# Performance work log

Hardware: AMD Instinct MI355X
Metric: run time of the kernel (lower is better)

The kernel has to match this reference:

```python
import jax, jax.numpy as jnp
import numpy as np

N = 100000   # nodes
E = 1600000  # edges (edge_index1)
F_IN = 53    # num_features_xd
D1 = 128     # output_dim1
D2 = 64      # output_dim2
G = 512      # graphs in batch


def setup_inputs() -> dict:
    key = jax.random.key(0)
    ks = jax.random.split(key, 16)
    kaiming = lambda k, fi, fo: jax.random.normal(k, (fi, fo), jnp.float32) * np.float32(np.sqrt(2.0 / fi))
    glorot = lambda k, fi, fo: jax.random.normal(k, (fi, fo), jnp.float32) * np.float32(np.sqrt(1.0 / fi))
    return {
        "x": jax.random.normal(ks[0], (N, F_IN), jnp.float32),
        "edge_inter": jax.random.randint(ks[1], (2, E), 0, N),
        "edge_intra": jax.random.randint(ks[2], (2, E), 0, N),
        "batch": jnp.sort(jax.random.randint(ks[3], (N,), 0, G)),
        "num_graphs": G,
        "w1": kaiming(ks[4], F_IN, D1), "b1": jnp.zeros((D1,), jnp.float32),
        "w2": kaiming(ks[5], D1, D2), "b2": jnp.zeros((D2,), jnp.float32),
        "gat_w": glorot(ks[6], D2, D2),
        "att_src": jax.random.normal(ks[7], (D2,), jnp.float32) * 0.1,
        "att_dst": jax.random.normal(ks[8], (D2,), jnp.float32) * 0.1,
        "gat_b": jnp.zeros((D2,), jnp.float32),
        "gcn_w": glorot(ks[9], D2, 2 * D2), "gcn_b": jnp.zeros((2 * D2,), jnp.float32),
        "fc1_w": glorot(ks[10], 2 * D2, 512), "fc1_b": jnp.zeros((512,), jnp.float32),
        "fc2_w": glorot(ks[11], 512, 256), "fc2_b": jnp.zeros((256,), jnp.float32),
        "out_w": glorot(ks[12], 256, 1), "out_b": jnp.zeros((1,), jnp.float32),
    }


def reference(x, edge_inter, edge_intra, batch, num_graphs,
              w1, b1, w2, b2, gat_w, att_src, att_dst, gat_b,
              gcn_w, gcn_b, fc1_w, fc1_b, fc2_w, fc2_b, out_w, out_b):
    n = x.shape[0]
    # node_embed: two dense layers + relu
    h = jax.nn.relu(x @ w1 + b1)
    h = jax.nn.relu(h @ w2 + b2)

    # add self-loops (PyG default for GATConv and GCNConv)
    loops = jnp.arange(n)
    src = jnp.concatenate([edge_inter[0], loops])  # message source j
    dst = jnp.concatenate([edge_inter[1], loops])  # message target i

    # ---- GATConv (heads=1): gather -> score -> edge softmax -> scatter ----
    hp = h @ gat_w                           # [N, D2]
    a_s = hp @ att_src                       # [N]
    a_d = hp @ att_dst                       # [N]
    e = jax.nn.leaky_relu(a_s[src] + a_d[dst], negative_slope=0.2)  # [E+N]
    emax = jax.ops.segment_max(e, dst, num_segments=n)
    ee = jnp.exp(e - emax[dst])
    denom = jax.ops.segment_sum(ee, dst, num_segments=n)
    alpha = ee / denom[dst]                  # edge softmax per target node
    h = jax.ops.segment_sum(alpha[:, None] * hp[src], dst, num_segments=n) + gat_b
    h = jax.nn.relu(h)

    # ---- GCNConv: symmetric-normalized sparse aggregation ----
    hw = h @ gcn_w                           # [N, 2*D2]
    deg = jax.ops.segment_sum(jnp.ones_like(e), dst, num_segments=n)
    d_inv = jnp.where(deg > 0, deg ** -0.5, 0.0)
    norm = d_inv[src] * d_inv[dst]           # [E+N]
    h = jax.ops.segment_sum(norm[:, None] * hw[src], dst, num_segments=n) + gcn_b
    h = jax.nn.relu(h)

    # ---- global max pool over graphs ----
    g = jax.ops.segment_max(h, batch, num_segments=num_graphs)
    g = jnp.maximum(g, 0.0)  # guard empty segments (-inf); h >= 0 after relu

    # ---- MLP head (dropout is identity in eval mode) ----
    z = jax.nn.relu(g @ fc1_w + fc1_b)
    z = jax.nn.relu(z @ fc2_w + fc2_b)
    return z @ out_w + out_b
```

## Files before the change

### kernel.cpp

```cpp
#include <hip/hip_runtime.h>
#include <hip/hip_bf16.h>

#define F_IN 53
#define D1   128
#define D2   64
#define D3   128
#define H1SZ 512
#define H2SZ 256

#define BUKSZ   256
#define BUKMAX  512
#define CAP     5120
#define PART_CH 4096

__global__ void k_vecproj(const float* __restrict__ gat_w,
                          const float* __restrict__ att_src,
                          const float* __restrict__ att_dst,
                          float* __restrict__ v_src, float* __restrict__ v_dst) {
    int k = threadIdx.x;
    float as = 0.f, ad = 0.f;
    #pragma unroll
    for (int c = 0; c < D2; ++c) {
        float w = gat_w[k * D2 + c];
        as = fmaf(w, att_src[c], as);
        ad = fmaf(w, att_dst[c], ad);
    }
    v_src[k] = as;
    v_dst[k] = ad;
}

__global__ __launch_bounds__(256) void k_embed(const float* __restrict__ x,
                                               const float* __restrict__ w1,
                                               const float* __restrict__ b1,
                                               const float* __restrict__ w2,
                                               const float* __restrict__ b2,
                                               const float* __restrict__ gat_w,
                                               const float* __restrict__ v_src,
                                               const float* __restrict__ v_dst,
                                               float* __restrict__ hp,
                                               float* __restrict__ a_s,
                                               float* __restrict__ a_d, int N) {
    __shared__ __align__(16) float xs[32][56];
    __shared__ __align__(16) float h1s[32][D1];
    __shared__ __align__(16) float h2s[32][D2];
    int tid = threadIdx.x;
    int n0 = blockIdx.x * 32;
    for (int i = tid; i < 32 * F_IN; i += 256) {
        int node = i / F_IN, kk = i - node * F_IN;
        xs[node][kk] = x[(size_t)n0 * F_IN + i];
    }
    __syncthreads();
    int c = tid & 63, grp = tid >> 6;
    int nb = grp * 8;
    {
        float acc0[8], acc1[8];
        float bb0 = b1[c], bb1 = b1[c + 64];
        #pragma unroll
        for (int j = 0; j < 8; ++j) { acc0[j] = bb0; acc1[j] = bb1; }
        #pragma unroll 1
        for (int kc = 0; kc < 13; ++kc) {
            int k4 = kc * 4;
            float wa0 = w1[(k4 + 0) * D1 + c];
            float wa1 = w1[(k4 + 1) * D1 + c];
            float wa2 = w1[(k4 + 2) * D1 + c];
            float wa3 = w1[(k4 + 3) * D1 + c];
            float wb0 = w1[(k4 + 0) * D1 + c + 64];
            float wb1 = w1[(k4 + 1) * D1 + c + 64];
            float wb2 = w1[(k4 + 2) * D1 + c + 64];
            float wb3 = w1[(k4 + 3) * D1 + c + 64];
            #pragma unroll
            for (int j = 0; j < 8; ++j) {
                float4 xv = *reinterpret_cast<const float4*>(&xs[nb + j][k4]);
                acc0[j] = fmaf(xv.x, wa0, acc0[j]);
                acc0[j] = fmaf(xv.y, wa1, acc0[j]);
                acc0[j] = fmaf(xv.z, wa2, acc0[j]);
                acc0[j] = fmaf(xv.w, wa3, acc0[j]);
                acc1[j] = fmaf(xv.x, wb0, acc1[j]);
                acc1[j] = fmaf(xv.y, wb1, acc1[j]);
                acc1[j] = fmaf(xv.z, wb2, acc1[j]);
                acc1[j] = fmaf(xv.w, wb3, acc1[j]);
            }
        }
        {
            float wa = w1[52 * D1 + c], wb = w1[52 * D1 + c + 64];
            #pragma unroll
            for (int j = 0; j < 8; ++j) {
                float xv = xs[nb + j][52];
                acc0[j] = fmaf(xv, wa, acc0[j]);
                acc1[j] = fmaf(xv, wb, acc1[j]);
            }
        }
        #pragma unroll
        for (int j = 0; j < 8; ++j) {
            h1s[nb + j][c]      = fmaxf(acc0[j], 0.f);
            h1s[nb + j][c + 64] = fmaxf(acc1[j], 0.f);
        }
    }
    float h2v[8];
    {
        float bb = b2[c];
        #pragma unroll
        for (int j = 0; j < 8; ++j) h2v[j] = bb;
        #pragma unroll 1
        for (int kc = 0; kc < 32; ++kc) {
            int k4 = kc * 4;
            float w0 = w2[(k4 + 0) * D2 + c];
            float w1v = w2[(k4 + 1) * D2 + c];
            float w2v = w2[(k4 + 2) * D2 + c];
            float w3v = w2[(k4 + 3) * D2 + c];
            #pragma unroll
            for (int j = 0; j < 8; ++j) {
                float4 hv = *reinterpret_cast<const float4*>(&h1s[nb + j][k4]);
                h2v[j] = fmaf(hv.x, w0, h2v[j]);
                h2v[j] = fmaf(hv.y, w1v, h2v[j]);
                h2v[j] = fmaf(hv.z, w2v, h2v[j]);
                h2v[j] = fmaf(hv.w, w3v, h2v[j]);
            }
        }
        #pragma unroll
        for (int j = 0; j < 8; ++j) {
            float v = fmaxf(h2v[j], 0.f);
            h2v[j] = v;
            h2s[nb + j][c] = v;
        }
    }
    {
        float vs = v_src[c], vd = v_dst[c];
        #pragma unroll
        for (int j = 0; j < 8; ++j) {
            float ps = h2v[j] * vs, pd = h2v[j] * vd;
            #pragma unroll
            for (int off = 32; off; off >>= 1) {
                ps += __shfl_down(ps, off);
                pd += __shfl_down(pd, off);
            }
            if (c == 0) { int n = n0 + nb + j; a_s[n] = ps; a_d[n] = pd; }
        }
    }
    {
        float acc[8];
        #pragma unroll
        for (int j = 0; j < 8; ++j) acc[j] = 0.f;
        #pragma unroll 1
        for (int kc = 0; kc < 16; ++kc) {
            int k4 = kc * 4;
            float w0 = gat_w[(k4 + 0) * D2 + c];
            float w1v = gat_w[(k4 + 1) * D2 + c];
            float w2v = gat_w[(k4 + 2) * D2 + c];
            float w3v = gat_w[(k4 + 3) * D2 + c];
            #pragma unroll
            for (int j = 0; j < 8; ++j) {
                float4 hv = *reinterpret_cast<const float4*>(&h2s[nb + j][k4]);
                acc[j] = fmaf(hv.x, w0, acc[j]);
                acc[j] = fmaf(hv.y, w1v, acc[j]);
                acc[j] = fmaf(hv.z, w2v, acc[j]);
                acc[j] = fmaf(hv.w, w3v, acc[j]);
            }
        }
        #pragma unroll
        for (int j = 0; j < 8; ++j)
            hp[(size_t)(n0 + nb + j) * D2 + c] = acc[j];
    }
}

__global__ __launch_bounds__(256) void k_part(const int* __restrict__ ei,
                                              int* __restrict__ gcount,
                                              int2* __restrict__ tmp,
                                              int E, int NBUK) {
    __shared__ int hist[BUKMAX];
    int tid = threadIdx.x;
    for (int i = tid; i < NBUK; i += 256) hist[i] = 0;
    __syncthreads();
    int k0 = blockIdx.x * PART_CH;
    int ss[16], dd[16];
    #pragma unroll
    for (int i = 0; i < 16; ++i) {
        int k = k0 + i * 256 + tid;
        if (k < E) {
            ss[i] = ei[k];
            dd[i] = ei[E + k];
            atomicAdd(&hist[dd[i] >> 8], 1);
        } else {
            dd[i] = -1;
        }
    }
    __syncthreads();
    for (int b = tid; b < NBUK; b += 256) {
        int c = hist[b];
        if (c > 0) hist[b] = b * CAP + atomicAdd(&gcount[b], c);
    }
    __syncthreads();
    #pragma unroll
    for (int i = 0; i < 16; ++i) {
        if (dd[i] >= 0) {
            int b = dd[i] >> 8;
            int pos = atomicAdd(&hist[b], 1);
            if (pos < (b + 1) * CAP) tmp[pos] = make_int2(ss[i], dd[i]);
        }
    }
}

__global__ __launch_bounds__(512) void k_bscan(const int* __restrict__ gcount,
                                               int* __restrict__ ebase, int NBUK) {
    __shared__ int sc[512];
    int t = threadIdx.x;
    int v = (t < NBUK) ? min(gcount[t], CAP) : 0;
    sc[t] = v;
    __syncthreads();
    #pragma unroll
    for (int off = 1; off < 512; off <<= 1) {
        int u = (t >= off) ? sc[t - off] : 0;
        __syncthreads();
        sc[t] += u;
        __syncthreads();
    }
    if (t < NBUK) ebase[t] = sc[t] - v;
}

__global__ __launch_bounds__(256) void k_build(const int2* __restrict__ tmp,
                                               const int* __restrict__ gcount,
                                               const int* __restrict__ ebase,
                                               int* __restrict__ offs,
                                               int* __restrict__ degi,
                                               float* __restrict__ dinv,
                                               int* __restrict__ csr_src, int N) {
    __shared__ int ldeg[256];
    __shared__ int lsc[256];
    __shared__ int lcur[256];
    int tid = threadIdx.x;
    int b = blockIdx.x;
    int n0 = b * BUKSZ;
    int nvalid = min(BUKSZ, N - n0);
    int cnt = min(gcount[b], CAP);
    int base = ebase[b] + n0;
    ldeg[tid] = 0;
    __syncthreads();
    for (int i = tid; i < cnt; i += 256) {
        int2 e = tmp[b * CAP + i];
        atomicAdd(&ldeg[e.y & 255], 1);
    }
    __syncthreads();
    int d = (tid < nvalid) ? (ldeg[tid] + 1) : 0;
    lsc[tid] = d;
    __syncthreads();
    #pragma unroll
    for (int off = 1; off < 256; off <<= 1) {
        int u = (tid >= off) ? lsc[tid - off] : 0;
        __syncthreads();
        lsc[tid] += u;
        __syncthreads();
    }
    int excl = lsc[tid] - d;
    if (tid < nvalid) {
        int n = n0 + tid;
        offs[n] = base + excl;
        degi[n] = d;
        dinv[n] = rsqrtf((float)d);
        lcur[tid] = excl;
    }
    __syncthreads();
    for (int i = tid; i < cnt; i += 256) {
        int2 e = tmp[b * CAP + i];
        int nl = e.y & 255;
        int r = atomicAdd(&lcur[nl], 1);
        csr_src[base + r] = e.x;
    }
    __syncthreads();
    if (tid < nvalid) {
        int r = atomicAdd(&lcur[tid], 1);
        csr_src[base + r] = n0 + tid;
    }
}

__global__ __launch_bounds__(256) void k_gat(const int* __restrict__ csr_src,
                                             const int* __restrict__ offs,
                                             const int* __restrict__ degi,
                                             const float* __restrict__ a_s,
                                             const float* __restrict__ a_d,
                                             const float* __restrict__ hp,
                                             const float* __restrict__ gat_b,
                                             const float* __restrict__ dinv,
                                             float* __restrict__ hscaled, int N) {
    __shared__ float ac[4][128];
    int wv = threadIdx.x >> 6, lane = threadIdx.x & 63;
    int node = blockIdx.x * 4 + wv;
    if (node >= N) return;
    int start = offs[node], deg = degi[node];
    float adn = a_d[node];
    float m = -1e30f, ssum = 0.f;
    for (int p = lane; p < deg; p += 64) {
        int s = csr_src[start + p];
        float e = a_s[s] + adn;
        e = (e > 0.f) ? e : 0.2f * e;
        float mn = fmaxf(m, e);
        ssum = ssum * __expf(m - mn) + __expf(e - mn);
        m = mn;
    }
    #pragma unroll
    for (int off = 32; off; off >>= 1) {
        float om = __shfl_xor(m, off);
        float os = __shfl_xor(ssum, off);
        float mn = fmaxf(m, om);
        ssum = ssum * __expf(m - mn) + os * __expf(om - mn);
        m = mn;
    }
    float rinv = 1.0f / ssum;
    int dcap = min(deg, 128);
    for (int p = lane; p < dcap; p += 64) {
        int s = csr_src[start + p];
        float e = a_s[s] + adn;
        e = (e > 0.f) ? e : 0.2f * e;
        ac[wv][p] = __expf(e - m) * rinv;
    }
    float acc = 0.f;
    int p = 0;
    for (; p + 8 <= dcap; p += 8) {
        int b = start + p;
        int s0 = csr_src[b + 0], s1 = csr_src[b + 1];
        int s2 = csr_src[b + 2], s3 = csr_src[b + 3];
        int s4 = csr_src[b + 4], s5 = csr_src[b + 5];
        int s6 = csr_src[b + 6], s7 = csr_src[b + 7];
        float v0 = hp[(size_t)s0 * D2 + lane];
        float v1 = hp[(size_t)s1 * D2 + lane];
        float v2 = hp[(size_t)s2 * D2 + lane];
        float v3 = hp[(size_t)s3 * D2 + lane];
        float v4 = hp[(size_t)s4 * D2 + lane];
        float v5 = hp[(size_t)s5 * D2 + lane];
        float v6 = hp[(size_t)s6 * D2 + lane];
        float v7 = hp[(size_t)s7 * D2 + lane];
        float b0 = fmaf(ac[wv][p + 0], v0, fmaf(ac[wv][p + 1], v1, 0.f));
        float b1 = fmaf(ac[wv][p + 2], v2, fmaf(ac[wv][p + 3], v3, 0.f));
        float b2 = fmaf(ac[wv][p + 4], v4, fmaf(ac[wv][p + 5], v5, 0.f));
        float b3 = fmaf(ac[wv][p + 6], v6, fmaf(ac[wv][p + 7], v7, 0.f));
        acc += (b0 + b1) + (b2 + b3);
    }
    for (; p < dcap; ++p) {
        int s = csr_src[start + p];
        acc = fmaf(ac[wv][p], hp[(size_t)s * D2 + lane], acc);
    }
    for (; p < deg; ++p) {
        int s = csr_src[start + p];
        float e = a_s[s] + adn;
        e = (e > 0.f) ? e : 0.2f * e;
        acc = fmaf(__expf(e - m) * rinv, hp[(size_t)s * D2 + lane], acc);
    }
    hscaled[(size_t)node * D2 + lane] = dinv[node] * fmaxf(acc + gat_b[lane], 0.f);
}

__global__ __launch_bounds__(256) void k_gcn(const int* __restrict__ csr_src,
                                             const int* __restrict__ offs,
                                             const int* __restrict__ degi,
                                             const float* __restrict__ dinv,
                                             const float* __restrict__ hscaled,
                                             float* __restrict__ hagg, int N) {
    int node = blockIdx.x * 4 + (threadIdx.x >> 6);
    int lane = threadIdx.x & 63;
    if (node >= N) return;
    int start = offs[node], deg = degi[node];
    float acc = 0.f;
    int p = 0;
    for (; p + 8 <= deg; p += 8) {
        int b = start + p;
        int s0 = csr_src[b + 0], s1 = csr_src[b + 1];
        int s2 = csr_src[b + 2], s3 = csr_src[b + 3];
        int s4 = csr_src[b + 4], s5 = csr_src[b + 5];
        int s6 = csr_src[b + 6], s7 = csr_src[b + 7];
        float v0 = hscaled[(size_t)s0 * D2 + lane];
        float v1 = hscaled[(size_t)s1 * D2 + lane];
        float v2 = hscaled[(size_t)s2 * D2 + lane];
        float v3 = hscaled[(size_t)s3 * D2 + lane];
        float v4 = hscaled[(size_t)s4 * D2 + lane];
        float v5 = hscaled[(size_t)s5 * D2 + lane];
        float v6 = hscaled[(size_t)s6 * D2 + lane];
        float v7 = hscaled[(size_t)s7 * D2 + lane];
        acc += ((v0 + v1) + (v2 + v3)) + ((v4 + v5) + (v6 + v7));
    }
    for (; p < deg; ++p) {
        int s = csr_src[start + p];
        acc += hscaled[(size_t)s * D2 + lane];
    }
    hagg[(size_t)node * D2 + lane] = acc * dinv[node];
}

__global__ void k_bounds(const int* __restrict__ batch, int* __restrict__ gstart,
                         int N, int G) {
    int n = blockIdx.x * blockDim.x + threadIdx.x;
    if (n >= N) return;
    int b = batch[n];
    if (n == 0) {
        for (int g = 0; g <= b; ++g) gstart[g] = 0;
    } else {
        int pb = batch[n - 1];
        for (int g = pb + 1; g <= b; ++g) gstart[g] = n;
    }
    if (n == N - 1) {
        for (int g = b + 1; g <= G; ++g) gstart[g] = N;
    }
}

__global__ __launch_bounds__(512) void k_pool(const float* __restrict__ hagg,
                                              const float* __restrict__ gcn_w,
                                              const float* __restrict__ gcn_b,
                                              const int* __restrict__ gstart,
                                              float* __restrict__ g) {
    __shared__ float ws[D2 * D3];
    __shared__ __align__(16) float rows[16 * D2];
    __shared__ float red[512];
    int tid = threadIdx.x;
    int gi = blockIdx.x;
    for (int i = tid; i < D2 * D3; i += 512) ws[i] = gcn_w[i];
    int ns = gstart[gi], ne = gstart[gi + 1];
    int col = tid & 127, grp = tid >> 7;
    float bias = gcn_b[col];
    float runmax = 0.f;
    for (int base = ns; base < ne; base += 16) {
        int cnt = min(16, ne - base);
        __syncthreads();
        for (int i = tid; i < cnt * D2; i += 512)
            rows[i] = hagg[(size_t)base * D2 + i];
        __syncthreads();
        int nb = grp * 4;
        float a0 = bias, a1 = bias, a2 = bias, a3 = bias;
        #pragma unroll 4
        for (int kc = 0; kc < 16; ++kc) {
            int k4 = kc * 4;
            float w0 = ws[(k4 + 0) * D3 + col];
            float w1v = ws[(k4 + 1) * D3 + col];
            float w2v = ws[(k4 + 2) * D3 + col];
            float w3v = ws[(k4 + 3) * D3 + col];
            float4 r0 = *reinterpret_cast<const float4*>(&rows[(nb + 0) * D2 + k4]);
            float4 r1 = *reinterpret_cast<const float4*>(&rows[(nb + 1) * D2 + k4]);
            float4 r2 = *reinterpret_cast<const float4*>(&rows[(nb + 2) * D2 + k4]);
            float4 r3 = *reinterpret_cast<const float4*>(&rows[(nb + 3) * D2 + k4]);
            a0 = fmaf(r0.x, w0, a0); a0 = fmaf(r0.y, w1v, a0);
            a0 = fmaf(r0.z, w2v, a0); a0 = fmaf(r0.w, w3v, a0);
            a1 = fmaf(r1.x, w0, a1); a1 = fmaf(r1.y, w1v, a1);
            a1 = fmaf(r1.z, w2v, a1); a1 = fmaf(r1.w, w3v, a1);
            a2 = fmaf(r2.x, w0, a2); a2 = fmaf(r2.y, w1v, a2);
            a2 = fmaf(r2.z, w2v, a2); a2 = fmaf(r2.w, w3v, a2);
            a3 = fmaf(r3.x, w0, a3); a3 = fmaf(r3.y, w1v, a3);
            a3 = fmaf(r3.z, w2v, a3); a3 = fmaf(r3.w, w3v, a3);
        }
        if (nb + 0 < cnt) runmax = fmaxf(runmax, a0);
        if (nb + 1 < cnt) runmax = fmaxf(runmax, a1);
        if (nb + 2 < cnt) runmax = fmaxf(runmax, a2);
        if (nb + 3 < cnt) runmax = fmaxf(runmax, a3);
    }
    red[tid] = runmax;
    __syncthreads();
    if (tid < 128) {
        float v = fmaxf(fmaxf(red[tid], red[tid + 128]),
                        fmaxf(red[tid + 256], red[tid + 384]));
        g[(size_t)gi * D3 + tid] = v;
    }
}

__global__ __launch_bounds__(512) void k_fc1(const float* __restrict__ g,
                                             const float* __restrict__ w,
                                             const float* __restrict__ b,
                                             float* __restrict__ z1) {
    __shared__ float gs[4 * D3];
    int t = threadIdx.x;
    int g0 = blockIdx.x * 4;
    if (t < 4 * D3) gs[t] = g[(size_t)g0 * D3 + t];
    __syncthreads();
    float bias = b[t];
    float a0 = bias, a1 = bias, a2 = bias, a3 = bias;
    for (int k = 0; k < D3; ++k) {
        float wv = w[k * H1SZ + t];
        a0 = fmaf(gs[k], wv, a0);
        a1 = fmaf(gs[D3 + k], wv, a1);
        a2 = fmaf(gs[2 * D3 + k], wv, a2);
        a3 = fmaf(gs[3 * D3 + k], wv, a3);
    }
    z1[(size_t)(g0 + 0) * H1SZ + t] = fmaxf(a0, 0.f);
    z1[(size_t)(g0 + 1) * H1SZ + t] = fmaxf(a1, 0.f);
    z1[(size_t)(g0 + 2) * H1SZ + t] = fmaxf(a2, 0.f);
    z1[(size_t)(g0 + 3) * H1SZ + t] = fmaxf(a3, 0.f);
}

__global__ __launch_bounds__(256) void k_fc2(const float* __restrict__ z1,
                                             const float* __restrict__ w,
                                             const float* __restrict__ b,
                                             float* __restrict__ z2) {
    __shared__ float zs[4 * H1SZ];
    int t = threadIdx.x;
    int g0 = blockIdx.x * 4;
    for (int i = t; i < 4 * H1SZ; i += 256) zs[i] = z1[(size_t)g0 * H1SZ + i];
    __syncthreads();
    float bias = b[t];
    float a0 = bias, a1 = bias, a2 = bias, a3 = bias;
    for (int k = 0; k < H1SZ; ++k) {
        float wv = w[k * H2SZ + t];
        a0 = fmaf(zs[k], wv, a0);
        a1 = fmaf(zs[H1SZ + k], wv, a1);
        a2 = fmaf(zs[2 * H1SZ + k], wv, a2);
        a3 = fmaf(zs[3 * H1SZ + k], wv, a3);
    }
    z2[(size_t)(g0 + 0) * H2SZ + t] = fmaxf(a0, 0.f);
    z2[(size_t)(g0 + 1) * H2SZ + t] = fmaxf(a1, 0.f);
    z2[(size_t)(g0 + 2) * H2SZ + t] = fmaxf(a2, 0.f);
    z2[(size_t)(g0 + 3) * H2SZ + t] = fmaxf(a3, 0.f);
}

__global__ __launch_bounds__(256) void k_out(const float* __restrict__ z2,
                                             const float* __restrict__ out_w,
                                             const float* __restrict__ out_b,
                                             float* __restrict__ out) {
    __shared__ float red[4];
    int gi = blockIdx.x, t = threadIdx.x;
    float p = z2[(size_t)gi * H2SZ + t] * out_w[t];
    #pragma unroll
    for (int off = 32; off; off >>= 1) p += __shfl_down(p, off);
    int lane = t & 63, w = t >> 6;
    if (lane == 0) red[w] = p;
    __syncthreads();
    if (t == 0) out[gi] = red[0] + red[1] + red[2] + red[3] + out_b[0];
}

extern "C" void kernel_launch(void* const* d_in, const int* in_sizes, int n_in,
                              void* d_out, int out_size, void* d_ws, size_t ws_size,
                              hipStream_t stream) {
    const float* x        = (const float*)d_in[0];
    const int*   ei       = (const int*)d_in[1];
    const int*   batch    = (const int*)d_in[3];
    const float* w1       = (const float*)d_in[5];
    const float* b1       = (const float*)d_in[6];
    const float* w2       = (const float*)d_in[7];
    const float* b2       = (const float*)d_in[8];
    const float* gat_w    = (const float*)d_in[9];
    const float* att_src  = (const float*)d_in[10];
    const float* att_dst  = (const float*)d_in[11];
    const float* gat_b    = (const float*)d_in[12];
    const float* gcn_w    = (const float*)d_in[13];
    const float* gcn_b    = (const float*)d_in[14];
    const float* fc1_w    = (const float*)d_in[15];
    const float* fc1_b    = (const float*)d_in[16];
    const float* fc2_w    = (const float*)d_in[17];
    const float* fc2_b    = (const float*)d_in[18];
    const float* out_w    = (const float*)d_in[19];
    const float* out_b    = (const float*)d_in[20];
    float* out = (float*)d_out;

    const int N = in_sizes[0] / F_IN;
    const int E = in_sizes[1] / 2;
    const int M = E + N;
    const int G = out_size;
    const int NBUK = (N + BUKSZ - 1) / BUKSZ;

    char* p = (char*)d_ws;
    size_t off = 0;
    auto alloc = [&](size_t bytes) { void* q = p + off; off += (bytes + 255) & ~(size_t)255; return q; };
    int2*  tmp     = (int2*)alloc((size_t)NBUK * CAP * 8);
    int*   csr_src = (int*)alloc((size_t)M * 4);
    float* hp      = (float*)alloc((size_t)N * D2 * 4);
    float* hscaled = (float*)alloc((size_t)N * D2 * 4);
    float* hagg    = (float*)alloc((size_t)N * D2 * 4);
    int*   offs    = (int*)alloc((size_t)N * 4);
    int*   degi    = (int*)alloc((size_t)N * 4);
    float* dinv    = (float*)alloc((size_t)N * 4);
    float* a_s     = (float*)alloc((size_t)N * 4);
    float* a_d     = (float*)alloc((size_t)N * 4);
    int*   gcount  = (int*)alloc((size_t)NBUK * 4);
    int*   ebase   = (int*)alloc((size_t)NBUK * 4);
    int*   gstart  = (int*)alloc((size_t)(G + 1) * 4);
    float* g       = (float*)alloc((size_t)G * D3 * 4);
    float* z1      = (float*)alloc((size_t)G * H1SZ * 4);
    float* z2      = (float*)alloc((size_t)G * H2SZ * 4);
    float* v_src   = (float*)alloc(D2 * 4);
    float* v_dst   = (float*)alloc(D2 * 4);

    hipMemsetAsync(gcount, 0, (size_t)NBUK * 4, stream);

    k_vecproj<<<1, 64, 0, stream>>>(gat_w, att_src, att_dst, v_src, v_dst);
    k_part<<<(E + PART_CH - 1) / PART_CH, 256, 0, stream>>>(ei, gcount, tmp, E, NBUK);
    k_embed<<<N / 32, 256, 0, stream>>>(x, w1, b1, w2, b2, gat_w, v_src, v_dst,
                                        hp, a_s, a_d, N);
    k_bscan<<<1, 512, 0, stream>>>(gcount, ebase, NBUK);
    k_build<<<NBUK, 256, 0, stream>>>(tmp, gcount, ebase, offs, degi, dinv, csr_src, N);
    k_bounds<<<(N + 255) / 256, 256, 0, stream>>>(batch, gstart, N, G);
    k_gat<<<(N + 3) / 4, 256, 0, stream>>>(csr_src, offs, degi, a_s, a_d, hp,
                                           gat_b, dinv, hscaled, N);
    k_gcn<<<(N + 3) / 4, 256, 0, stream>>>(csr_src, offs, degi, dinv, hscaled, hagg, N);
    k_pool<<<G, 512, 0, stream>>>(hagg, gcn_w, gcn_b, gstart, g);
    k_fc1<<<G / 4, 512, 0, stream>>>(g, fc1_w, fc1_b, z1);
    k_fc2<<<G / 4, 256, 0, stream>>>(z1, fc2_w, fc2_b, z2);
    k_out<<<G, 256, 0, stream>>>(z2, out_w, out_b, out);
}
```

Before: 393.8 us.

## Fuse embed, edge partition and graph bounds into one launch; widen gather batches

Merges the node-embedding, edge partition and graph-bounds kernels into one launch by dispatching on block index, with shared memory overlaid through a union. The separate bucket-scan kernel is dropped, and each build block now recomputes its prefix offset with a reduction over gcount. In the GAT kernel, attention logits are cached in LDS during the online softmax pass so the source indices and a_s values are not re-read. Both the GAT and GCN gathers now batch 16 loads at a time with clamped indices to raise memory-level parallelism. This cuts launch overhead and redundant reads, at the cost of extra predicated work and some redundant prefix computation per block.

```diff
diff --git a/kernel.cpp b/kernel.cpp
--- a/kernel.cpp
+++ b/kernel.cpp
@@ -29,7 +29,7 @@
     v_dst[k] = ad;
 }
 
-__global__ __launch_bounds__(256) void k_embed(const float* __restrict__ x,
+__global__ __launch_bounds__(256) void k_fused(const float* __restrict__ x,
                                                const float* __restrict__ w1,
                                                const float* __restrict__ b1,
                                                const float* __restrict__ w2,
@@ -39,15 +39,74 @@
                                                const float* __restrict__ v_dst,
                                                float* __restrict__ hp,
                                                float* __restrict__ a_s,
-                                               float* __restrict__ a_d, int N) {
-    __shared__ __align__(16) float xs[32][56];
-    __shared__ __align__(16) float h1s[32][D1];
-    __shared__ __align__(16) float h2s[32][D2];
+                                               float* __restrict__ a_d,
+                                               const int* __restrict__ ei,
+                                               int* __restrict__ gcount,
+                                               int2* __restrict__ tmp,
+                                               const int* __restrict__ batch,
+                                               int* __restrict__ gstart,
+                                               int N, int E, int NBUK, int G,
+                                               int embB, int partB) {
+    __shared__ __align__(16) union {
+        struct { float xs[32][56]; float h1s[32][D1]; float h2s[32][D2]; } e;
+        int hist[BUKMAX];
+    } sm;
     int tid = threadIdx.x;
-    int n0 = blockIdx.x * 32;
+    int bid = blockIdx.x;
+
+    if (bid >= embB) {
+        if (bid < embB + partB) {
+            for (int i = tid; i < NBUK; i += 256) sm.hist[i] = 0;
+            __syncthreads();
+            int k0 = (bid - embB) * PART_CH;
+            int ss[16], dd[16];
+            #pragma unroll
+            for (int i = 0; i < 16; ++i) {
+                int k = k0 + i * 256 + tid;
+                if (k < E) {
+                    ss[i] = ei[k];
+                    dd[i] = ei[E + k];
+                    atomicAdd(&sm.hist[dd[i] >> 8], 1);
+                } else {
+                    dd[i] = -1;
+                }
+            }
+            __syncthreads();
+            for (int b = tid; b < NBUK; b += 256) {
+                int c = sm.hist[b];
+                if (c > 0) sm.hist[b] = b * CAP + atomicAdd(&gcount[b], c);
+            }
+            __syncthreads();
+            #pragma unroll
+            for (int i = 0; i < 16; ++i) {
+                if (dd[i] >= 0) {
+                    int b = dd[i] >> 8;
+                    int pos = atomicAdd(&sm.hist[b], 1);
+                    if (pos < (b + 1) * CAP) tmp[pos] = make_int2(ss[i], dd[i]);
+                }
+            }
+        } else {
+            int n = (bid - embB - partB) * 256 + tid;
+            if (n < N) {
+                int b = batch[n];
+                if (n == 0) {
+                    for (int g = 0; g <= b; ++g) gstart[g] = 0;
+                } else {
+                    int pb = batch[n - 1];
+                    for (int g = pb + 1; g <= b; ++g) gstart[g] = n;
+                }
+                if (n == N - 1) {
+                    for (int g = b + 1; g <= G; ++g) gstart[g] = N;
+                }
+            }
+        }
+        return;
+    }
+
+    int n0 = bid * 32;
     for (int i = tid; i < 32 * F_IN; i += 256) {
         int node = i / F_IN, kk = i - node * F_IN;
-        xs[node][kk] = x[(size_t)n0 * F_IN + i];
+        sm.e.xs[node][kk] = x[(size_t)n0 * F_IN + i];
     }
     __syncthreads();
     int c = tid & 63, grp = tid >> 6;
@@ -70,7 +129,7 @@
             float wb3 = w1[(k4 + 3) * D1 + c + 64];
             #pragma unroll
             for (int j = 0; j < 8; ++j) {
-                float4 xv = *reinterpret_cast<const float4*>(&xs[nb + j][k4]);
+                float4 xv = *reinterpret_cast<const float4*>(&sm.e.xs[nb + j][k4]);
                 acc0[j] = fmaf(xv.x, wa0, acc0[j]);
                 acc0[j] = fmaf(xv.y, wa1, acc0[j]);
                 acc0[j] = fmaf(xv.z, wa2, acc0[j]);
@@ -85,15 +144,15 @@
             float wa = w1[52 * D1 + c], wb = w1[52 * D1 + c + 64];
             #pragma unroll
             for (int j = 0; j < 8; ++j) {
-                float xv = xs[nb + j][52];
+                float xv = sm.e.xs[nb + j][52];
                 acc0[j] = fmaf(xv, wa, acc0[j]);
                 acc1[j] = fmaf(xv, wb, acc1[j]);
             }
         }
         #pragma unroll
         for (int j = 0; j < 8; ++j) {
-            h1s[nb + j][c]      = fmaxf(acc0[j], 0.f);
-            h1s[nb + j][c + 64] = fmaxf(acc1[j], 0.f);
+            sm.e.h1s[nb + j][c]      = fmaxf(acc0[j], 0.f);
+            sm.e.h1s[nb + j][c + 64] = fmaxf(acc1[j], 0.f);
         }
     }
     float h2v[8];
@@ -110,7 +169,7 @@
             float w3v = w2[(k4 + 3) * D2 + c];
             #pragma unroll
             for (int j = 0; j < 8; ++j) {
-                float4 hv = *reinterpret_cast<const float4*>(&h1s[nb + j][k4]);
+                float4 hv = *reinterpret_cast<const float4*>(&sm.e.h1s[nb + j][k4]);
                 h2v[j] = fmaf(hv.x, w0, h2v[j]);
                 h2v[j] = fmaf(hv.y, w1v, h2v[j]);
                 h2v[j] = fmaf(hv.z, w2v, h2v[j]);
@@ -121,7 +180,7 @@
         for (int j = 0; j < 8; ++j) {
             float v = fmaxf(h2v[j], 0.f);
             h2v[j] = v;
-            h2s[nb + j][c] = v;
+            sm.e.h2s[nb + j][c] = v;
         }
     }
     {
@@ -150,7 +209,7 @@
             float w3v = gat_w[(k4 + 3) * D2 + c];
             #pragma unroll
             for (int j = 0; j < 8; ++j) {
-                float4 hv = *reinterpret_cast<const float4*>(&h2s[nb + j][k4]);
+                float4 hv = *reinterpret_cast<const float4*>(&sm.e.h2s[nb + j][k4]);
                 acc[j] = fmaf(hv.x, w0, acc[j]);
                 acc[j] = fmaf(hv.y, w1v, acc[j]);
                 acc[j] = fmaf(hv.z, w2v, acc[j]);
@@ -163,63 +222,8 @@
     }
 }
 
-__global__ __launch_bounds__(256) void k_part(const int* __restrict__ ei,
-                                              int* __restrict__ gcount,
-                                              int2* __restrict__ tmp,
-                                              int E, int NBUK) {
-    __shared__ int hist[BUKMAX];
-    int tid = threadIdx.x;
-    for (int i = tid; i < NBUK; i += 256) hist[i] = 0;
-    __syncthreads();
-    int k0 = blockIdx.x * PART_CH;
-    int ss[16], dd[16];
-    #pragma unroll
-    for (int i = 0; i < 16; ++i) {
-        int k = k0 + i * 256 + tid;
-        if (k < E) {
-            ss[i] = ei[k];
-            dd[i] = ei[E + k];
-            atomicAdd(&hist[dd[i] >> 8], 1);
-        } else {
-            dd[i] = -1;
-        }
-    }
-    __syncthreads();
-    for (int b = tid; b < NBUK; b += 256) {
-        int c = hist[b];
-        if (c > 0) hist[b] = b * CAP + atomicAdd(&gcount[b], c);
-    }
-    __syncthreads();
-    #pragma unroll
-    for (int i = 0; i < 16; ++i) {
-        if (dd[i] >= 0) {
-            int b = dd[i] >> 8;
-            int pos = atomicAdd(&hist[b], 1);
-            if (pos < (b + 1) * CAP) tmp[pos] = make_int2(ss[i], dd[i]);
-        }
-    }
-}
-
-__global__ __launch_bounds__(512) void k_bscan(const int* __restrict__ gcount,
-                                               int* __restrict__ ebase, int NBUK) {
-    __shared__ int sc[512];
-    int t = threadIdx.x;
-    int v = (t < NBUK) ? min(gcount[t], CAP) : 0;
-    sc[t] = v;
-    __syncthreads();
-    #pragma unroll
-    for (int off = 1; off < 512; off <<= 1) {
-        int u = (t >= off) ? sc[t - off] : 0;
-        __syncthreads();
-        sc[t] += u;
-        __syncthreads();
-    }
-    if (t < NBUK) ebase[t] = sc[t] - v;
-}
-
 __global__ __launch_bounds__(256) void k_build(const int2* __restrict__ tmp,
                                                const int* __restrict__ gcount,
-                                               const int* __restrict__ ebase,
                                                int* __restrict__ offs,
                                                int* __restrict__ degi,
                                                float* __restrict__ dinv,
@@ -227,14 +231,23 @@
     __shared__ int ldeg[256];
     __shared__ int lsc[256];
     __shared__ int lcur[256];
+    __shared__ int pref[256];
     int tid = threadIdx.x;
     int b = blockIdx.x;
     int n0 = b * BUKSZ;
     int nvalid = min(BUKSZ, N - n0);
     int cnt = min(gcount[b], CAP);
-    int base = ebase[b] + n0;
+    int acc = 0;
+    for (int i = tid; i < b; i += 256) acc += min(gcount[i], CAP);
+    pref[tid] = acc;
     ldeg[tid] = 0;
     __syncthreads();
+    #pragma unroll
+    for (int off = 128; off; off >>= 1) {
+        if (tid < off) pref[tid] += pref[tid + off];
+        __syncthreads();
+    }
+    int base = pref[0] + n0;
     for (int i = tid; i < cnt; i += 256) {
         int2 e = tmp[b * CAP + i];
         atomicAdd(&ldeg[e.y & 255], 1);
@@ -286,12 +299,14 @@
     int node = blockIdx.x * 4 + wv;
     if (node >= N) return;
     int start = offs[node], deg = degi[node];
+    int dcap = min(deg, 128);
     float adn = a_d[node];
     float m = -1e30f, ssum = 0.f;
     for (int p = lane; p < deg; p += 64) {
         int s = csr_src[start + p];
         float e = a_s[s] + adn;
         e = (e > 0.f) ? e : 0.2f * e;
+        if (p < 128) ac[wv][p] = e;
         float mn = fmaxf(m, e);
         ssum = ssum * __expf(m - mn) + __expf(e - mn);
         m = mn;
@@ -305,40 +320,25 @@
         m = mn;
     }
     float rinv = 1.0f / ssum;
-    int dcap = min(deg, 128);
-    for (int p = lane; p < dcap; p += 64) {
-        int s = csr_src[start + p];
-        float e = a_s[s] + adn;
-        e = (e > 0.f) ? e : 0.2f * e;
-        ac[wv][p] = __expf(e - m) * rinv;
-    }
+    if (lane < dcap)      ac[wv][lane]      = __expf(ac[wv][lane] - m) * rinv;
+    if (lane + 64 < dcap) ac[wv][lane + 64] = __expf(ac[wv][lane + 64] - m) * rinv;
     float acc = 0.f;
-    int p = 0;
-    for (; p + 8 <= dcap; p += 8) {
-        int b = start + p;
-        int s0 = csr_src[b + 0], s1 = csr_src[b + 1];
-        int s2 = csr_src[b + 2], s3 = csr_src[b + 3];
-        int s4 = csr_src[b + 4], s5 = csr_src[b + 5];
-        int s6 = csr_src[b + 6], s7 = csr_src[b + 7];
-        float v0 = hp[(size_t)s0 * D2 + lane];
-        float v1 = hp[(size_t)s1 * D2 + lane];
-        float v2 = hp[(size_t)s2 * D2 + lane];
-        float v3 = hp[(size_t)s3 * D2 + lane];
-        float v4 = hp[(size_t)s4 * D2 + lane];
-        float v5 = hp[(size_t)s5 * D2 + lane];
-        float v6 = hp[(size_t)s6 * D2 + lane];
-        float v7 = hp[(size_t)s7 * D2 + lane];
-        float b0 = fmaf(ac[wv][p + 0], v0, fmaf(ac[wv][p + 1], v1, 0.f));
-        float b1 = fmaf(ac[wv][p + 2], v2, fmaf(ac[wv][p + 3], v3, 0.f));
-        float b2 = fmaf(ac[wv][p + 4], v4, fmaf(ac[wv][p + 5], v5, 0.f));
-        float b3 = fmaf(ac[wv][p + 6], v6, fmaf(ac[wv][p + 7], v7, 0.f));
-        acc += (b0 + b1) + (b2 + b3);
-    }
-    for (; p < dcap; ++p) {
-        int s = csr_src[start + p];
-        acc = fmaf(ac[wv][p], hp[(size_t)s * D2 + lane], acc);
-    }
-    for (; p < deg; ++p) {
+    for (int pp = 0; pp < dcap; pp += 16) {
+        int s[16]; float w[16];
+        #pragma unroll
+        for (int i = 0; i < 16; ++i) {
+            int q = pp + i;
+            int qc = (q < dcap) ? q : (dcap - 1);
+            s[i] = csr_src[start + qc];
+            w[i] = (q < dcap) ? ac[wv][q] : 0.f;
+        }
+        float v[16];
+        #pragma unroll
+        for (int i = 0; i < 16; ++i) v[i] = hp[(size_t)s[i] * D2 + lane];
+        #pragma unroll
+        for (int i = 0; i < 16; ++i) acc = fmaf(w[i], v[i], acc);
+    }
+    for (int p = 128; p < deg; ++p) {
         int s = csr_src[start + p];
         float e = a_s[s] + adn;
         e = (e > 0.f) ? e : 0.2f * e;
@@ -358,44 +358,21 @@
     if (node >= N) return;
     int start = offs[node], deg = degi[node];
     float acc = 0.f;
-    int p = 0;
-    for (; p + 8 <= deg; p += 8) {
-        int b = start + p;
-        int s0 = csr_src[b + 0], s1 = csr_src[b + 1];
-        int s2 = csr_src[b + 2], s3 = csr_src[b + 3];
-        int s4 = csr_src[b + 4], s5 = csr_src[b + 5];
-        int s6 = csr_src[b + 6], s7 = csr_src[b + 7];
-        float v0 = hscaled[(size_t)s0 * D2 + lane];
-        float v1 = hscaled[(size_t)s1 * D2 + lane];
-        float v2 = hscaled[(size_t)s2 * D2 + lane];
-        float v3 = hscaled[(size_t)s3 * D2 + lane];
-        float v4 = hscaled[(size_t)s4 * D2 + lane];
-        float v5 = hscaled[(size_t)s5 * D2 + lane];
-        float v6 = hscaled[(size_t)s6 * D2 + lane];
-        float v7 = hscaled[(size_t)s7 * D2 + lane];
-        acc += ((v0 + v1) + (v2 + v3)) + ((v4 + v5) + (v6 + v7));
-    }
-    for (; p < deg; ++p) {
-        int s = csr_src[start + p];
-        acc += hscaled[(size_t)s * D2 + lane];
+    for (int pp = 0; pp < deg; pp += 16) {
+        int s[16];
+        #pragma unroll
+        for (int i = 0; i < 16; ++i) {
+            int q = pp + i;
+            int qc = (q < deg) ? q : (deg - 1);
+            s[i] = csr_src[start + qc];
+        }
+        float v[16];
+        #pragma unroll
+        for (int i = 0; i < 16; ++i) v[i] = hscaled[(size_t)s[i] * D2 + lane];
+        #pragma unroll
+        for (int i = 0; i < 16; ++i) acc += (pp + i < deg) ? v[i] : 0.f;
     }
     hagg[(size_t)node * D2 + lane] = acc * dinv[node];
-}
-
-__global__ void k_bounds(const int* __restrict__ batch, int* __restrict__ gstart,
-                         int N, int G) {
-    int n = blockIdx.x * blockDim.x + threadIdx.x;
-    if (n >= N) return;
-    int b = batch[n];
-    if (n == 0) {
-        for (int g = 0; g <= b; ++g) gstart[g] = 0;
-    } else {
-        int pb = batch[n - 1];
-        for (int g = pb + 1; g <= b; ++g) gstart[g] = n;
-    }
-    if (n == N - 1) {
-        for (int g = b + 1; g <= G; ++g) gstart[g] = N;
-    }
 }
 
 __global__ __launch_bounds__(512) void k_pool(const float* __restrict__ hagg,
@@ -547,6 +524,9 @@
     const int M = E + N;
     const int G = out_size;
     const int NBUK = (N + BUKSZ - 1) / BUKSZ;
+    const int embB   = N / 32;
+    const int partB  = (E + PART_CH - 1) / PART_CH;
+    const int boundB = (N + 255) / 256;
 
     char* p = (char*)d_ws;
     size_t off = 0;
@@ -562,7 +542,6 @@
     float* a_s     = (float*)alloc((size_t)N * 4);
     float* a_d     = (float*)alloc((size_t)N * 4);
     int*   gcount  = (int*)alloc((size_t)NBUK * 4);
-    int*   ebase   = (int*)alloc((size_t)NBUK * 4);
     int*   gstart  = (int*)alloc((size_t)(G + 1) * 4);
     float* g       = (float*)alloc((size_t)G * D3 * 4);
     float* z1      = (float*)alloc((size_t)G * H1SZ * 4);
@@ -573,12 +552,10 @@
     hipMemsetAsync(gcount, 0, (size_t)NBUK * 4, stream);
 
     k_vecproj<<<1, 64, 0, stream>>>(gat_w, att_src, att_dst, v_src, v_dst);
-    k_part<<<(E + PART_CH - 1) / PART_CH, 256, 0, stream>>>(ei, gcount, tmp, E, NBUK);
-    k_embed<<<N / 32, 256, 0, stream>>>(x, w1, b1, w2, b2, gat_w, v_src, v_dst,
-                                        hp, a_s, a_d, N);
-    k_bscan<<<1, 512, 0, stream>>>(gcount, ebase, NBUK);
-    k_build<<<NBUK, 256, 0, stream>>>(tmp, gcount, ebase, offs, degi, dinv, csr_src, N);
-    k_bounds<<<(N + 255) / 256, 256, 0, stream>>>(batch, gstart, N, G);
+    k_fused<<<embB + partB + boundB, 256, 0, stream>>>(
+        x, w1, b1, w2, b2, gat_w, v_src, v_dst, hp, a_s, a_d,
+        ei, gcount, tmp, batch, gstart, N, E, NBUK, G, embB, partB);
+    k_build<<<NBUK, 256, 0, stream>>>(tmp, gcount, offs, degi, dinv, csr_src, N);
     k_gat<<<(N + 3) / 4, 256, 0, stream>>>(csr_src, offs, degi, a_s, a_d, hp,
                                            gat_b, dinv, hscaled, N);
     k_gcn<<<(N + 3) / 4, 256, 0, stream>>>(csr_src, offs, degi, dinv, hscaled, hagg, N);
```

After: 345.0 us. 1.14x faster.
